# Optimization experiments

Hardware: AMD Instinct MI355X
Metric: run time of the kernel (lower is better)

Reference implementation:

```python
import jax, jax.numpy as jnp
import numpy as np

B, S, K, N = 4, 2048, 4096, 11008
GROUP_SIZE = 128
NUM_GROUPS = K // GROUP_SIZE  # 32


def setup_inputs() -> dict:
    key = jax.random.key(0)
    k1, k2, k3, k4, k5 = jax.random.split(key, 5)
    x = jax.random.normal(k1, (B, S, K), dtype=jnp.float32)
    # sensitivity-sorted column order is a permutation of [0, K)
    col_indices = jax.random.permutation(k2, K).astype(jnp.int32)
    # packed uint8 nibbles stored as int32 in [0, 256)
    w_packed = jax.random.randint(k3, (K // 2, N), 0, 256, dtype=jnp.int32)
    # per-group, per-output-column dequant scales (positive, small)
    scales = (jax.random.uniform(k4, (NUM_GROUPS, N), dtype=jnp.float32) + 0.05) * 0.01
    bias = jax.random.normal(k5, (N,), dtype=jnp.float32) * 0.01
    return {"x": x, "col_indices": col_indices, "w_packed": w_packed,
            "scales": scales, "bias": bias}


def _dequant_weight(w_packed, scales):
    # unpack int4 nibbles: low nibble -> even k, high nibble -> odd k
    low = (w_packed & 15) - 8          # [K//2, N]
    high = ((w_packed >> 4) & 15) - 8  # [K//2, N]
    w_int = jnp.stack([low, high], axis=1).reshape(K, N)  # interleaved [K, N]
    # per-group dequant: scale index = k // group_size
    w = w_int.astype(scales.dtype).reshape(NUM_GROUPS, GROUP_SIZE, N)
    w = w * scales[:, None, :]
    return w.reshape(K, N)


def reference(x, col_indices, w_packed, scales, bias):
    orig_shape = x.shape
    xm = x.reshape(-1, K)                     # [M, K]
    xg = jnp.take(xm, col_indices, axis=1)    # column-reorder gather [M, K]
    w = _dequant_weight(w_packed, scales)     # [K, N]
    out = jnp.einsum('mk,kn->mn', xg, w)      # fp32 accumulate
    out = out + bias
    return out.reshape(orig_shape[0], orig_shape[1], N)
```

## Files before the change

kernel.cpp:

```cpp
#include <hip/hip_runtime.h>
#include <hip/hip_bf16.h>
#include <stdint.h>

#define M_DIM 8192
#define K_DIM 4096
#define N_DIM 11008

typedef __attribute__((ext_vector_type(8))) short bf16x8;
typedef __attribute__((ext_vector_type(4))) float f32x4;
typedef __attribute__((ext_vector_type(4))) unsigned int uint4v;

__device__ __forceinline__ unsigned short f2bf(float f) {
    __hip_bfloat16 h = __float2bfloat16(f);
    return __builtin_bit_cast(unsigned short, h);
}

__device__ __forceinline__ void gload_lds16(const unsigned short* g, unsigned short* l) {
    __builtin_amdgcn_global_load_lds(
        (const __attribute__((address_space(1))) void*)g,
        (__attribute__((address_space(3))) void*)l,
        16, 0, 0);
}

__global__ void permute_x_kernel(const float* __restrict__ x,
                                 const int* __restrict__ ci,
                                 unsigned short* __restrict__ xg) {
    int idx = blockIdx.x * 256 + threadIdx.x;
    int64_t base = (int64_t)idx * 4;
    int m = (int)(base >> 12);
    int k = (int)(base & 4095);
    const float* xrow = x + ((int64_t)m << 12);
    int4 c4 = *reinterpret_cast<const int4*>(ci + k);
    ushort4 o;
    o.x = f2bf(xrow[c4.x]);
    o.y = f2bf(xrow[c4.y]);
    o.z = f2bf(xrow[c4.z]);
    o.w = f2bf(xrow[c4.w]);
    *reinterpret_cast<ushort4*>(xg + base) = o;
}

__global__ void dequant_w_kernel(const int* __restrict__ wp,
                                 const float* __restrict__ scales,
                                 unsigned short* __restrict__ wT) {
    __shared__ unsigned short tile[64][65];
    int n0 = blockIdx.x * 64;
    int k0 = blockIdx.y * 64;
    int g = k0 >> 7;
    int t = threadIdx.x;
    int col = t & 63;
    int r0 = t >> 6;
    float s = scales[(int64_t)g * N_DIM + n0 + col];
    int pr0 = k0 >> 1;
#pragma unroll
    for (int i = 0; i < 8; ++i) {
        int row = r0 + i * 4;
        int p = wp[(int64_t)(pr0 + row) * N_DIM + n0 + col];
        tile[2 * row][col]     = f2bf((float)((p & 15) - 8) * s);
        tile[2 * row + 1][col] = f2bf((float)(((p >> 4) & 15) - 8) * s);
    }
    __syncthreads();
    int nl = t >> 2;
    int kk0 = (t & 3) << 4;
    unsigned short vals[16];
#pragma unroll
    for (int j = 0; j < 16; ++j) vals[j] = tile[kk0 + j][nl];
    uint4v* dst = reinterpret_cast<uint4v*>(wT + (int64_t)(n0 + nl) * K_DIM + k0 + kk0);
    dst[0] = *reinterpret_cast<const uint4v*>(&vals[0]);
    dst[1] = *reinterpret_cast<const uint4v*>(&vals[8]);
}

__global__ void gemm_kernel(const unsigned short* __restrict__ A,
                            const unsigned short* __restrict__ BT,
                            const float* __restrict__ bias,
                            float* __restrict__ C) {
    __shared__ unsigned short As[128 * 64];
    __shared__ unsigned short Bs[128 * 64];

    constexpr int NTILES = N_DIM / 128;
    int wg = blockIdx.x;
    int nwg = gridDim.x;
    int q = nwg >> 3, r = nwg & 7;
    int xcd = wg & 7, li = wg >> 3;
    int swz = (xcd < r ? xcd * (q + 1) : r * (q + 1) + (xcd - r) * q) + li;
    int by = swz / NTILES;
    int bx = swz - by * NTILES;
    int brow = by << 7, bcol = bx << 7;

    int t = threadIdx.x;
    int lane = t & 63;
    int wid = t >> 6;
    int wr = wid >> 1, wc = wid & 1;
    int fr = lane & 15, fq = lane >> 4;

    f32x4 acc[4][4];
#pragma unroll
    for (int m = 0; m < 4; ++m)
#pragma unroll
        for (int n = 0; n < 4; ++n) acc[m][n] = (f32x4){0.f, 0.f, 0.f, 0.f};

    int srow = t >> 3;
    int scol = (t & 7) << 3;
    const unsigned short* aSrc = A + (int64_t)(brow + srow) * K_DIM + scol;
    const unsigned short* bSrc = BT + (int64_t)(bcol + srow) * K_DIM + scol;
    unsigned short* aDst = As + srow * 64 + scol;
    unsigned short* bDst = Bs + srow * 64 + scol;

    const unsigned short* aRd = As + (wr * 64 + fr) * 64 + fq * 8;
    const unsigned short* bRd = Bs + (wc * 64 + fr) * 64 + fq * 8;

    for (int kt = 0; kt < K_DIM / 64; ++kt) {
        __syncthreads();
#pragma unroll
        for (int i = 0; i < 4; ++i) {
            gload_lds16(aSrc + i * 32 * K_DIM, aDst + i * 32 * 64);
            gload_lds16(bSrc + i * 32 * K_DIM, bDst + i * 32 * 64);
        }
        __syncthreads();
#pragma unroll
        for (int kk = 0; kk < 2; ++kk) {
            bf16x8 av[4], bv[4];
#pragma unroll
            for (int m = 0; m < 4; ++m)
                av[m] = *reinterpret_cast<const bf16x8*>(aRd + m * 16 * 64 + kk * 32);
#pragma unroll
            for (int n = 0; n < 4; ++n)
                bv[n] = *reinterpret_cast<const bf16x8*>(bRd + n * 16 * 64 + kk * 32);
#pragma unroll
            for (int m = 0; m < 4; ++m)
#pragma unroll
                for (int n = 0; n < 4; ++n)
                    acc[m][n] = __builtin_amdgcn_mfma_f32_16x16x32_bf16(
                        av[m], bv[n], acc[m][n], 0, 0, 0);
        }
        aSrc += 64;
        bSrc += 64;
    }

    int orow0 = brow + wr * 64 + fq * 4;
    int ocol0 = bcol + wc * 64 + fr;
#pragma unroll
    for (int n = 0; n < 4; ++n) {
        int col = ocol0 + n * 16;
        float bval = bias[col];
#pragma unroll
        for (int m = 0; m < 4; ++m) {
            int row = orow0 + m * 16;
            float* cp = C + (int64_t)row * N_DIM + col;
#pragma unroll
            for (int j = 0; j < 4; ++j) {
                cp[(int64_t)j * N_DIM] = acc[m][n][j] + bval;
            }
        }
    }
}

extern "C" void kernel_launch(void* const* d_in, const int* in_sizes, int n_in,
                              void* d_out, int out_size, void* d_ws, size_t ws_size,
                              hipStream_t stream) {
    const float* x      = (const float*)d_in[0];
    const int* ci       = (const int*)d_in[1];
    const int* wp       = (const int*)d_in[2];
    const float* scales = (const float*)d_in[3];
    const float* bias   = (const float*)d_in[4];
    float* out          = (float*)d_out;

    const size_t wT_bytes = (size_t)N_DIM * K_DIM * 2;
    unsigned short* wT = (unsigned short*)d_ws;
    unsigned short* xg = wT + (size_t)N_DIM * K_DIM;

    size_t cap = (ws_size > wT_bytes) ? (ws_size - wT_bytes) : 0;
    int max_rows = (int)(cap / ((size_t)K_DIM * 2));
    int chunk_rows = (max_rows / 128) * 128;
    if (chunk_rows <= 0) chunk_rows = 128;
    if (chunk_rows > M_DIM) chunk_rows = M_DIM;

    dequant_w_kernel<<<dim3(N_DIM / 64, K_DIM / 64), 256, 0, stream>>>(wp, scales, wT);

    for (int m0 = 0; m0 < M_DIM; m0 += chunk_rows) {
        int rows = M_DIM - m0 < chunk_rows ? M_DIM - m0 : chunk_rows;
        int pgrid = (int)(((int64_t)rows * K_DIM) / (4 * 256));
        permute_x_kernel<<<pgrid, 256, 0, stream>>>(
            x + (int64_t)m0 * K_DIM, ci, xg);
        int grid = (rows / 128) * (N_DIM / 128);
        gemm_kernel<<<grid, 256, 0, stream>>>(
            xg, wT, bias, out + (int64_t)m0 * N_DIM);
    }
}
```

Baseline: 1.000 ms.

## Rewrite GEMM as 256x256 double-buffered 8-wave pipeline with staged LDS loads

Replaces the 128x128, 4-wave GEMM with a 256x256 tile computed by 8 waves, each holding an 8x4 block of 16x16 accumulators. The kernel uses two LDS buffers (128KB total) filled by global_load_lds. Loads for later k-tiles are interleaved with MFMA blocks, and progress is tracked with explicit vmcnt waits, barriers and s_setprio. The goal is to hide global memory latency behind compute and to raise reuse per LDS byte, removing the load-then-sync stall of the old single-buffered loop. The cost is a large LDS footprint, heavy register pressure, and brittle hand-counted wait counts that must match the issue order.

```diff
diff --git a/kernel.cpp b/kernel.cpp
--- a/kernel.cpp
+++ b/kernel.cpp
@@ -5,6 +5,8 @@
 #define M_DIM 8192
 #define K_DIM 4096
 #define N_DIM 11008
+#define NKT   (K_DIM / 64)
+#define NIT   (NKT / 2)
 
 typedef __attribute__((ext_vector_type(8))) short bf16x8;
 typedef __attribute__((ext_vector_type(4))) float f32x4;
@@ -69,81 +71,163 @@
     dst[1] = *reinterpret_cast<const uint4v*>(&vals[8]);
 }
 
-__global__ void gemm_kernel(const unsigned short* __restrict__ A,
-                            const unsigned short* __restrict__ BT,
-                            const float* __restrict__ bias,
-                            float* __restrict__ C) {
-    __shared__ unsigned short As[128 * 64];
-    __shared__ unsigned short Bs[128 * 64];
-
-    constexpr int NTILES = N_DIM / 128;
-    int wg = blockIdx.x;
-    int nwg = gridDim.x;
+
+template <int BUF, int KK, int MB>
+__device__ __forceinline__ void lda4(bf16x8 (&d)[8], const unsigned short* lds, int aBase) {
+#pragma unroll
+    for (int m = 0; m < 4; ++m)
+        d[MB + m] = *reinterpret_cast<const bf16x8*>(
+            lds + BUF * 32768 + KK * 8192 + aBase + (MB + m) * 512);
+}
+
+template <int BUF, int KK>
+__device__ __forceinline__ void ldb4(bf16x8 (&d)[4], const unsigned short* lds, int bBase) {
+#pragma unroll
+    for (int n = 0; n < 4; ++n)
+        d[n] = *reinterpret_cast<const bf16x8*>(
+            lds + BUF * 32768 + 16384 + KK * 8192 + bBase + n * 512);
+}
+
+template <int MB>
+__device__ __forceinline__ void mfma_blk(f32x4 (&acc)[8][4], const bf16x8 (&av)[8],
+                                         const bf16x8 (&bv)[4]) {
+    __builtin_amdgcn_s_setprio(1);
+#pragma unroll
+    for (int m = 0; m < 4; ++m)
+#pragma unroll
+        for (int n = 0; n < 4; ++n)
+            acc[MB + m][n] = __builtin_amdgcn_mfma_f32_16x16x32_bf16(
+                av[MB + m], bv[n], acc[MB + m][n], 0, 0, 0);
+    __builtin_amdgcn_s_setprio(0);
+}
+
+template <int BUF, int ISB, int KK>
+__device__ __forceinline__ void stage(const unsigned short* __restrict__ G, int row0,
+                                      int kt, unsigned short* lds,
+                                      int w32, int riw, int s8, int wLds) {
+    if (kt < NKT) {
+#pragma unroll
+        for (int j = 0; j < 2; ++j) {
+            const unsigned short* src =
+                G + (int64_t)(row0 + w32 + j * 16 + riw) * K_DIM + kt * 64 + KK * 32 + s8;
+            gload_lds16(src, lds + BUF * 32768 + ISB * 16384 + KK * 8192 + wLds + j * 512);
+        }
+    }
+}
+
+#define BAR() do { __builtin_amdgcn_s_barrier(); asm volatile("" ::: "memory"); } while (0)
+
+__global__ __launch_bounds__(512, 2)
+void gemm_kernel(const unsigned short* __restrict__ A,
+                 const unsigned short* __restrict__ BT,
+                 const float* __restrict__ bias,
+                 float* __restrict__ C) {
+    __shared__ unsigned short lds[65536];
+
+    constexpr int NT = N_DIM / 256;
+    int wg = blockIdx.x, nwg = gridDim.x;
     int q = nwg >> 3, r = nwg & 7;
     int xcd = wg & 7, li = wg >> 3;
     int swz = (xcd < r ? xcd * (q + 1) : r * (q + 1) + (xcd - r) * q) + li;
-    int by = swz / NTILES;
-    int bx = swz - by * NTILES;
-    int brow = by << 7, bcol = bx << 7;
+    int by = swz / NT, bx = swz - by * NT;
+    int brow = by << 8, bcol = bx << 8;
 
     int t = threadIdx.x;
-    int lane = t & 63;
-    int wid = t >> 6;
-    int wr = wid >> 1, wc = wid & 1;
+    int lane = t & 63, w = t >> 6;
+    int wr = w >> 2, wc = w & 3;
     int fr = lane & 15, fq = lane >> 4;
 
-    f32x4 acc[4][4];
-#pragma unroll
-    for (int m = 0; m < 4; ++m)
+    const int aBase = (wr * 128 + fr) * 32 + fq * 8;
+    const int bBase = (wc * 64 + fr) * 32 + fq * 8;
+    const int riw = lane >> 2, s8 = (lane & 3) << 3;
+    const int w32 = w * 32, wLds = w * 1024;
+
+    f32x4 acc[8][4];
+#pragma unroll
+    for (int m = 0; m < 8; ++m)
 #pragma unroll
         for (int n = 0; n < 4; ++n) acc[m][n] = (f32x4){0.f, 0.f, 0.f, 0.f};
 
-    int srow = t >> 3;
-    int scol = (t & 7) << 3;
-    const unsigned short* aSrc = A + (int64_t)(brow + srow) * K_DIM + scol;
-    const unsigned short* bSrc = BT + (int64_t)(bcol + srow) * K_DIM + scol;
-    unsigned short* aDst = As + srow * 64 + scol;
-    unsigned short* bDst = Bs + srow * 64 + scol;
-
-    const unsigned short* aRd = As + (wr * 64 + fr) * 64 + fq * 8;
-    const unsigned short* bRd = Bs + (wc * 64 + fr) * 64 + fq * 8;
-
-    for (int kt = 0; kt < K_DIM / 64; ++kt) {
-        __syncthreads();
-#pragma unroll
-        for (int i = 0; i < 4; ++i) {
-            gload_lds16(aSrc + i * 32 * K_DIM, aDst + i * 32 * 64);
-            gload_lds16(bSrc + i * 32 * K_DIM, bDst + i * 32 * 64);
-        }
-        __syncthreads();
-#pragma unroll
-        for (int kk = 0; kk < 2; ++kk) {
-            bf16x8 av[4], bv[4];
-#pragma unroll
-            for (int m = 0; m < 4; ++m)
-                av[m] = *reinterpret_cast<const bf16x8*>(aRd + m * 16 * 64 + kk * 32);
-#pragma unroll
-            for (int n = 0; n < 4; ++n)
-                bv[n] = *reinterpret_cast<const bf16x8*>(bRd + n * 16 * 64 + kk * 32);
-#pragma unroll
-            for (int m = 0; m < 4; ++m)
-#pragma unroll
-                for (int n = 0; n < 4; ++n)
-                    acc[m][n] = __builtin_amdgcn_mfma_f32_16x16x32_bf16(
-                        av[m], bv[n], acc[m][n], 0, 0, 0);
-        }
-        aSrc += 64;
-        bSrc += 64;
-    }
-
-    int orow0 = brow + wr * 64 + fq * 4;
+    stage<0, 0, 0>(A,  brow, 0, lds, w32, riw, s8, wLds);
+    stage<0, 0, 1>(A,  brow, 0, lds, w32, riw, s8, wLds);
+    stage<0, 1, 0>(BT, bcol, 0, lds, w32, riw, s8, wLds);
+    stage<0, 1, 1>(BT, bcol, 0, lds, w32, riw, s8, wLds);
+    stage<1, 1, 0>(BT, bcol, 1, lds, w32, riw, s8, wLds);
+    stage<1, 0, 0>(A,  brow, 1, lds, w32, riw, s8, wLds);
+    stage<1, 1, 1>(BT, bcol, 1, lds, w32, riw, s8, wLds);
+    asm volatile("s_waitcnt vmcnt(6)" ::: "memory");
+    BAR();
+
+#pragma unroll 1
+    for (int it = 0; it < NIT; ++it) {
+        const int t1 = 2 * it + 1, t2 = 2 * it + 2, t3 = 2 * it + 3;
+        const bool lastIt = (it == NIT - 1);
+        bf16x8 a0[8], a1[8], b0[4], b1[4];
+
+        lda4<0, 0, 0>(a0, lds, aBase);
+        ldb4<0, 0>(b0, lds, bBase);
+        stage<1, 0, 1>(A, brow, t1, lds, w32, riw, s8, wLds);
+        BAR();
+        mfma_blk<0>(acc, a0, b0);
+        BAR();
+
+        lda4<0, 0, 4>(a0, lds, aBase);
+        lda4<0, 1, 0>(a1, lds, aBase);
+        stage<0, 1, 0>(BT, bcol, t2, lds, w32, riw, s8, wLds);
+        BAR();
+        mfma_blk<4>(acc, a0, b0);
+        BAR();
+
+        lda4<0, 1, 4>(a1, lds, aBase);
+        ldb4<0, 1>(b1, lds, bBase);
+        stage<0, 0, 0>(A, brow, t2, lds, w32, riw, s8, wLds);
+        BAR();
+        mfma_blk<0>(acc, a1, b1);
+        BAR();
+
+        stage<0, 1, 1>(BT, bcol, t2, lds, w32, riw, s8, wLds);
+        BAR();
+        mfma_blk<4>(acc, a1, b1);
+        if (!lastIt) asm volatile("s_waitcnt vmcnt(6)" ::: "memory");
+        else         asm volatile("s_waitcnt vmcnt(0)" ::: "memory");
+        BAR();
+
+        lda4<1, 0, 0>(a0, lds, aBase);
+        ldb4<1, 0>(b0, lds, bBase);
+        stage<0, 0, 1>(A, brow, t2, lds, w32, riw, s8, wLds);
+        BAR();
+        mfma_blk<0>(acc, a0, b0);
+        BAR();
+
+        lda4<1, 0, 4>(a0, lds, aBase);
+        lda4<1, 1, 0>(a1, lds, aBase);
+        stage<1, 1, 0>(BT, bcol, t3, lds, w32, riw, s8, wLds);
+        BAR();
+        mfma_blk<4>(acc, a0, b0);
+        BAR();
+
+        lda4<1, 1, 4>(a1, lds, aBase);
+        ldb4<1, 1>(b1, lds, bBase);
+        stage<1, 0, 0>(A, brow, t3, lds, w32, riw, s8, wLds);
+        BAR();
+        mfma_blk<0>(acc, a1, b1);
+        BAR();
+
+        stage<1, 1, 1>(BT, bcol, t3, lds, w32, riw, s8, wLds);
+        BAR();
+        mfma_blk<4>(acc, a1, b1);
+        if (!lastIt) asm volatile("s_waitcnt vmcnt(6)" ::: "memory");
+        BAR();
+    }
+
+    int orow0 = brow + wr * 128 + fq * 4;
     int ocol0 = bcol + wc * 64 + fr;
 #pragma unroll
     for (int n = 0; n < 4; ++n) {
         int col = ocol0 + n * 16;
         float bval = bias[col];
 #pragma unroll
-        for (int m = 0; m < 4; ++m) {
+        for (int m = 0; m < 8; ++m) {
             int row = orow0 + m * 16;
             float* cp = C + (int64_t)row * N_DIM + col;
 #pragma unroll
@@ -170,8 +254,8 @@
 
     size_t cap = (ws_size > wT_bytes) ? (ws_size - wT_bytes) : 0;
     int max_rows = (int)(cap / ((size_t)K_DIM * 2));
-    int chunk_rows = (max_rows / 128) * 128;
-    if (chunk_rows <= 0) chunk_rows = 128;
+    int chunk_rows = (max_rows / 256) * 256;
+    if (chunk_rows <= 0) chunk_rows = 256;
     if (chunk_rows > M_DIM) chunk_rows = M_DIM;
 
     dequant_w_kernel<<<dim3(N_DIM / 64, K_DIM / 64), 256, 0, stream>>>(wp, scales, wT);
@@ -181,8 +265,8 @@
         int pgrid = (int)(((int64_t)rows * K_DIM) / (4 * 256));
         permute_x_kernel<<<pgrid, 256, 0, stream>>>(
             x + (int64_t)m0 * K_DIM, ci, xg);
-        int grid = (rows / 128) * (N_DIM / 128);
-        gemm_kernel<<<grid, 256, 0, stream>>>(
+        int grid = (rows / 256) * (N_DIM / 256);
+        gemm_kernel<<<grid, 512, 0, stream>>>(
             xg, wT, bias, out + (int64_t)m0 * N_DIM);
     }
 }
```

Result: faster. 902.0 us (-9.8%).
